# Optimization experiments

Hardware: AMD Instinct MI355X
Metric: run time of the kernel (lower is better)

Reference implementation:

```python
import jax, jax.numpy as jnp
import numpy as np

B, S, D, H = 8, 1024, 1024, 16
DK = D // H


def setup_inputs() -> dict:
    key = jax.random.key(0)
    ks = jax.random.split(key, 12)
    sc = 1.0 / np.sqrt(D)
    return {
        "query": jax.random.normal(ks[0], (B, S, D), jnp.float32),
        "key": jax.random.normal(ks[1], (B, S, D), jnp.float32),
        "value": jax.random.normal(ks[2], (B, S, D), jnp.float32),
        "Wq": jax.random.normal(ks[3], (D, D), jnp.float32) * sc,
        "bq": jnp.zeros((D,), jnp.float32),
        "Wk": jax.random.normal(ks[4], (D, D), jnp.float32) * sc,
        "bk": jnp.zeros((D,), jnp.float32),
        "Wv": jax.random.normal(ks[5], (D, D), jnp.float32) * sc,
        "bv": jnp.zeros((D,), jnp.float32),
        "Wa": jax.random.normal(ks[6], (D, D), jnp.float32) * sc,
        "ba": jnp.zeros((D,), jnp.float32),
        "qvec": jax.random.normal(ks[7], (D,), jnp.float32),
    }


def reference(query, key, value, Wq, bq, Wk, bk, Wv, bv, Wa, ba, qvec):
    # project and split heads: [B,S,D] -> [B,H,S,DK]
    def split(x, W, b):
        y = x @ W.T + b
        return y.reshape(B, S, H, DK).transpose(0, 2, 1, 3)

    q = split(query, Wq, bq)
    k = split(key, Wk, bk)
    v = split(value, Wv, bv)

    scores = jnp.einsum('bhqd,bhkd->bhqk', q, k) / jnp.sqrt(jnp.float32(DK))
    p = jax.nn.softmax(scores, axis=-1)          # dropout p=0 -> identity
    x = jnp.einsum('bhqk,bhkd->bhqd', p, v)
    x = x.transpose(0, 2, 1, 3).reshape(B, S, D)  # [B,S,D]

    # attention2 pooling head
    a = jnp.tanh(x @ Wa.T + ba) @ qvec           # [B,S]
    alpha = jax.nn.softmax(a, axis=-1)
    return jnp.einsum('bs,bsd->bd', alpha, x)    # [B,D]
```

## Files before the change

### kernel.cpp

```cpp
#include <hip/hip_runtime.h>

typedef __bf16 bf16;
typedef __attribute__((ext_vector_type(8))) __bf16 bf16x8;
typedef __attribute__((ext_vector_type(4))) __bf16 bf16x4;
typedef __attribute__((ext_vector_type(4))) float f32x4;

#define GLDS16(g, l) __builtin_amdgcn_global_load_lds( \
    (const __attribute__((address_space(1))) void*)(g), \
    (__attribute__((address_space(3))) void*)(l), 16, 0, 0)

#define MFMA16(a, b, c) __builtin_amdgcn_mfma_f32_16x16x32_bf16(a, b, c, 0, 0, 0)

#define TR16(dst, addr, off) \
  asm volatile("ds_read_b64_tr_b16 %0, %1 offset:" #off : "=v"(dst) : "v"(addr))

struct CvtAll { const float* in[7]; bf16* out[7]; };

__global__ __launch_bounds__(256) void f2b_all(CvtAll a) {
  const int i = blockIdx.x * 256 + threadIdx.x;
  const float* in;
  bf16* out;
  int off;
  if (blockIdx.y < 3) {
    in = a.in[blockIdx.y];
    out = a.out[blockIdx.y];
    off = i;
  } else {
    if (i >= 524288) return;
    const int widx = 3 + (i >> 17);
    in = a.in[widx];
    out = a.out[widx];
    off = i & 131071;
  }
  const f32x4* p = (const f32x4*)in + (size_t)off * 2;
  f32x4 x = p[0], y = p[1];
  bf16x8 o;
  o[0] = (bf16)x[0]; o[1] = (bf16)x[1]; o[2] = (bf16)x[2]; o[3] = (bf16)x[3];
  o[4] = (bf16)y[0]; o[5] = (bf16)y[1]; o[6] = (bf16)y[2]; o[7] = (bf16)y[3];
  ((bf16x8*)out)[off] = o;
}

template <int EPI, int MF>
__device__ __forceinline__ void gemm_body8(
    const bf16* __restrict__ A, const bf16* __restrict__ Bw,
    const float* __restrict__ bias, const float* __restrict__ qv,
    bf16* __restrict__ C, float* __restrict__ part,
    const int row0, const int col0, const int N, const int K) {
  constexpr int BM = MF * 32;
  constexpr int ASZ = MF * 1024;
  constexpr int BUF = 2 * ASZ + 16384;
  constexpr int RSH = (MF == 8) ? 8 : 7;
  __shared__ __attribute__((aligned(16))) bf16 L[2 * BUF];
  const int tid = threadIdx.x;
  const int wid = tid >> 6, lane = tid & 63;
  const int g = lane >> 4, lc = lane & 15;
  const int wr = wid >> 2, wc = wid & 3;

  const bf16* gA = A + (size_t)(row0 + (tid & (BM - 1))) * K + (tid >> RSH) * 8;
  const bf16* gB = Bw + (size_t)(col0 + (tid & 255)) * K + (tid >> 8) * 8;
  const int d0 = (tid - lane) * 8;

#define STG_A(T, kh) do { \
    const bf16* gp_ = gA + (T) * 64 + (kh) * 32; \
    bf16* lp_ = L + ((T) & 1) * BUF + (kh) * ASZ + d0; \
    GLDS16(gp_, lp_); \
    if constexpr (MF == 8) GLDS16(gp_ + 16, lp_ + 4096); } while (0)
#define STG_B(T, kh) do { \
    const bf16* gp_ = gB + (T) * 64 + (kh) * 32; \
    bf16* lp_ = L + ((T) & 1) * BUF + 2 * ASZ + (kh) * 8192 + d0; \
    GLDS16(gp_, lp_); GLDS16(gp_ + 16, lp_ + 4096); } while (0)
#define RD_A(c, kh) do { \
    _Pragma("unroll") for (int m_ = 0; m_ < MF; ++m_) \
      af[m_] = *(const bf16x8*)&L[(c) * BUF + (kh) * ASZ + g * (BM * 8) + \
                                  (wr * (MF * 16) + m_ * 16 + lc) * 8]; \
  } while (0)
#define RD_B(c, kh, nh) do { \
    bf[0] = *(const bf16x8*)&L[(c) * BUF + 2 * ASZ + (kh) * 8192 + g * 2048 + \
                               (wc * 64 + (nh) * 32 + lc) * 8]; \
    bf[1] = *(const bf16x8*)&L[(c) * BUF + 2 * ASZ + (kh) * 8192 + g * 2048 + \
                               (wc * 64 + (nh) * 32 + 16 + lc) * 8]; \
  } while (0)
#define BARS \
    __builtin_amdgcn_s_barrier(); \
    asm volatile("s_waitcnt lgkmcnt(0)" ::: "memory"); \
    __builtin_amdgcn_sched_barrier(0);
#define MM(nh) do { \
    __builtin_amdgcn_s_setprio(1); \
    _Pragma("unroll") for (int m_ = 0; m_ < MF; ++m_) { \
      acc[m_][(nh) * 2 + 0] = MFMA16(af[m_], bf[0], acc[m_][(nh) * 2 + 0]); \
      acc[m_][(nh) * 2 + 1] = MFMA16(af[m_], bf[1], acc[m_][(nh) * 2 + 1]); \
    } \
    __builtin_amdgcn_s_setprio(0); } while (0)
#define ENDP do { \
    __builtin_amdgcn_s_barrier(); \
    asm volatile("" ::: "memory"); \
    __builtin_amdgcn_sched_barrier(0); } while (0)
#define VGATE() do { \
    if constexpr (MF == 8) { asm volatile("s_waitcnt vmcnt(6)" ::: "memory"); } \
    else                   { asm volatile("s_waitcnt vmcnt(4)" ::: "memory"); } } while (0)

  const f32x4 z4 = {0.f, 0.f, 0.f, 0.f};
  f32x4 acc[MF][4];
#pragma unroll
  for (int m = 0; m < MF; ++m)
#pragma unroll
    for (int n = 0; n < 4; ++n) acc[m][n] = z4;

  bf16x8 af[MF], bf[2];
  const int NT = K >> 6;
  const int NI = NT >> 1;

  STG_A(0, 0); STG_B(0, 0); STG_A(0, 1); STG_B(0, 1);
  STG_A(1, 0); STG_B(1, 0); STG_A(1, 1);
  VGATE();
  ENDP;

  for (int i = 0; i < NI; ++i) {
    const int t1 = 2 * i + 1, t2 = 2 * i + 2, t3 = 2 * i + 3;
    const bool p2 = t2 < NT, p3 = t3 < NT;
    RD_A(0, 0); RD_B(0, 0, 0);
    STG_B(t1, 1);
    BARS; MM(0); ENDP;
    RD_B(0, 0, 1);
    if (p2) STG_A(t2, 0);
    BARS; MM(1); ENDP;
    RD_A(0, 1); RD_B(0, 1, 0);
    if (p2) STG_B(t2, 0);
    BARS; MM(0); ENDP;
    RD_B(0, 1, 1);
    if (p2) STG_A(t2, 1);
    BARS; MM(1);
    if (p2) { VGATE(); }
    else    { asm volatile("s_waitcnt vmcnt(0)" ::: "memory"); }
    ENDP;
    RD_A(1, 0); RD_B(1, 0, 0);
    if (p2) STG_B(t2, 1);
    BARS; MM(0); ENDP;
    RD_B(1, 0, 1);
    if (p3) STG_A(t3, 0);
    BARS; MM(1); ENDP;
    RD_A(1, 1); RD_B(1, 1, 0);
    if (p3) STG_B(t3, 0);
    BARS; MM(0); ENDP;
    RD_B(1, 1, 1);
    if (p3) STG_A(t3, 1);
    BARS; MM(1);
    VGATE();
    ENDP;
  }

#undef STG_A
#undef STG_B
#undef RD_A
#undef RD_B
#undef BARS
#undef MM
#undef ENDP
#undef VGATE

  if constexpr (EPI == 0) {
#pragma unroll
    for (int n = 0; n < 4; ++n) {
      const int col = col0 + wc * 64 + n * 16 + lc;
      const float bb = bias[col];
#pragma unroll
      for (int m = 0; m < MF; ++m)
#pragma unroll
        for (int r = 0; r < 4; ++r) {
          const int row = row0 + wr * (MF * 16) + m * 16 + g * 4 + r;
          C[(size_t)row * N + col] = (bf16)(acc[m][n][r] + bb);
        }
    }
  } else {
    float ps[MF][4];
#pragma unroll
    for (int m = 0; m < MF; ++m)
#pragma unroll
      for (int r = 0; r < 4; ++r) ps[m][r] = 0.f;
#pragma unroll
    for (int n = 0; n < 4; ++n) {
      const int col = col0 + wc * 64 + n * 16 + lc;
      const float bb = bias[col];
      const float qq = qv[col];
#pragma unroll
      for (int m = 0; m < MF; ++m)
#pragma unroll
        for (int r = 0; r < 4; ++r)
          ps[m][r] += tanhf(acc[m][n][r] + bb) * qq;
    }
    float* pdst = part + (size_t)((col0 >> 8) * 4 + wc) * 8192;
#pragma unroll
    for (int m = 0; m < MF; ++m)
#pragma unroll
      for (int r = 0; r < 4; ++r) {
        float v = ps[m][r];
        v += __shfl_xor(v, 1); v += __shfl_xor(v, 2);
        v += __shfl_xor(v, 4); v += __shfl_xor(v, 8);
        if (lc == 0) {
          const int row = row0 + wr * (MF * 16) + m * 16 + g * 4 + r;
          pdst[row] = v;
        }
      }
  }
}

__device__ __forceinline__ void swz128(int phys, int& row0, int& col0) {
  const int lg = (phys & 7) * 16 + (phys >> 3);
  row0 = (lg >> 2) * 256;
  col0 = (lg & 3) * 256;
}

__device__ __forceinline__ void swz256(int phys, int& row0, int& col0) {
  const int lg = (phys & 7) * 32 + (phys >> 3);
  row0 = (lg >> 2) * 128;
  col0 = (lg & 3) * 256;
}

struct GemmSet { const bf16* A; const bf16* Bw; const float* bias; bf16* C; };
struct Gemm3Args { GemmSet s[3]; };

__global__ __launch_bounds__(512, 2) void gemm3_kernel(Gemm3Args a) {
  const GemmSet s = a.s[blockIdx.y];
  int row0, col0;
  swz128(blockIdx.x, row0, col0);
  gemm_body8<0, 8>(s.A, s.Bw, s.bias, nullptr, s.C, nullptr, row0, col0, 1024, 1024);
}

__global__ __launch_bounds__(512, 2) void gemm_a_kernel(
    const bf16* __restrict__ A, const bf16* __restrict__ Bw,
    const float* __restrict__ bias, const float* __restrict__ qv,
    float* __restrict__ part) {
  int row0, col0;
  swz256(blockIdx.x, row0, col0);
  gemm_body8<1, 4>(A, Bw, bias, qv, nullptr, part, row0, col0, 1024, 1024);
}

__global__ __launch_bounds__(256) void attn_kernel(
    const bf16* __restrict__ qp, const bf16* __restrict__ kp,
    const bf16* __restrict__ vp, bf16* __restrict__ xb, float* __restrict__ xf) {
  constexpr int S = 1024, D = 1024;
  __shared__ __attribute__((aligned(16))) bf16 Ks[8192];
  __shared__ __attribute__((aligned(16))) bf16 Vs[8192];
  __shared__ __attribute__((aligned(16))) bf16 Ps[8192];
  const int tid = threadIdx.x, wid = tid >> 6, lane = tid & 63;
  const int g = lane >> 4, lc = lane & 15;
  const int b = blockIdx.x >> 4, h = blockIdx.x & 15;
  const int q0 = blockIdx.y * 128;
  const size_t base = (size_t)b * S * D + (size_t)h * 64;

  bf16x8 qf[2][2];
#pragma unroll
  for (int qg = 0; qg < 2; ++qg) {
    const bf16* qrow = qp + base + (size_t)(q0 + qg * 64 + wid * 16 + lc) * D;
    qf[qg][0] = *(const bf16x8*)(qrow + g * 8);
    qf[qg][1] = *(const bf16x8*)(qrow + 32 + g * 8);
#pragma unroll
    for (int j = 0; j < 8; ++j) {
      qf[qg][0][j] = (bf16)((float)qf[qg][0][j] * 0.125f);
      qf[qg][1][j] = (bf16)((float)qf[qg][1][j] * 0.125f);
    }
  }
  float m_s[2] = {-1e30f, -1e30f}, l_s[2] = {0.f, 0.f};
  const f32x4 z4 = {0.f, 0.f, 0.f, 0.f};
  f32x4 ax[2][4];
#pragma unroll
  for (int qg = 0; qg < 2; ++qg)
#pragma unroll
    for (int m = 0; m < 4; ++m) ax[qg][m] = z4;

  const int c0 = tid, c1 = tid + 256;
  const bf16* gK0 = kp + base + (size_t)(c0 & 63) * D + (c0 >> 6) * 8;
  const bf16* gK1 = kp + base + (size_t)(c1 & 63) * D + (c1 >> 6) * 8;
  bf16* lK0 = Ks + (size_t)(c0 - lane) * 8;
  bf16* lK1 = Ks + (size_t)(c1 - lane) * 8;
  const bf16* gV0 = vp + base + (size_t)((c0 >> 5) * 4 + ((c0 >> 1) & 3)) * D +
                    ((c0 >> 3) & 3) * 16 + (c0 & 1) * 8;
  const bf16* gV1 = vp + base + (size_t)((c1 >> 5) * 4 + ((c1 >> 1) & 3)) * D +
                    ((c1 >> 3) & 3) * 16 + (c1 & 1) * 8;
  bf16* lV0 = Vs + (size_t)(c0 - lane) * 8;
  bf16* lV1 = Vs + (size_t)(c1 - lane) * 8;

  bf16* pw = Ps + wid * 2048;
  const int pswz_a = lc & 3, pswz_b = (lc >> 2) & 3;
  const unsigned vaddr0 =
      (unsigned)(uintptr_t)(const __attribute__((address_space(3))) bf16*)(Vs + 512 * g + 4 * lc);

  GLDS16(gK0, lK0);
  GLDS16(gK1, lK1);
  GLDS16(gV0, lV0);
  GLDS16(gV1, lV1);

  for (int t = 0; t < 16; ++t) {
    __syncthreads();
    const int cur = t & 1;
    if (t < 15) {
      const size_t off = (size_t)(t + 1) * 64 * D;
      const int nb = cur ^ 1;
      GLDS16(gK0 + off, lK0 + nb * 4096);
      GLDS16(gK1 + off, lK1 + nb * 4096);
      GLDS16(gV0 + off, lV0 + nb * 4096);
      GLDS16(gV1 + off, lV1 + nb * 4096);
    }
    const bf16* Kb = Ks + cur * 4096;
    const unsigned va = vaddr0 + cur * 8192u;

    bf16x4 vt[4][2][2];
    TR16(vt[0][0][0], va, 0);    TR16(vt[1][0][0], va, 128);
    TR16(vt[2][0][0], va, 256);  TR16(vt[3][0][0], va, 384);
    TR16(vt[0][0][1], va, 512);  TR16(vt[1][0][1], va, 640);
    TR16(vt[2][0][1], va, 768);  TR16(vt[3][0][1], va, 896);
    TR16(vt[0][1][0], va, 4096); TR16(vt[1][1][0], va, 4224);
    TR16(vt[2][1][0], va, 4352); TR16(vt[3][1][0], va, 4480);
    TR16(vt[0][1][1], va, 4608); TR16(vt[1][1][1], va, 4736);
    TR16(vt[2][1][1], va, 4864); TR16(vt[3][1][1], va, 4992);
    asm volatile("s_waitcnt lgkmcnt(0)" ::: "memory");
    __builtin_amdgcn_sched_barrier(0);

#pragma unroll
    for (int qg = 0; qg < 2; ++qg) {
      f32x4 sc[4];
      __builtin_amdgcn_s_setprio(1);
#pragma unroll
      for (int m = 0; m < 4; ++m) {
        f32x4 z = z4;
        bf16x8 kf0 = *(const bf16x8*)(Kb + (size_t)g * 512 + (m * 16 + lc) * 8);
        bf16x8 kf1 = *(const bf16x8*)(Kb + (size_t)(4 + g) * 512 + (m * 16 + lc) * 8);
        z = MFMA16(kf0, qf[qg][0], z);
        z = MFMA16(kf1, qf[qg][1], z);
        sc[m] = z;
      }
      __builtin_amdgcn_s_setprio(0);

      float mx = -1e30f;
#pragma unroll
      for (int m = 0; m < 4; ++m)
        mx = fmaxf(mx, fmaxf(fmaxf(sc[m][0], sc[m][1]), fmaxf(sc[m][2], sc[m][3])));
      mx = fmaxf(mx, __shfl_xor(mx, 16));
      mx = fmaxf(mx, __shfl_xor(mx, 32));
      if (!__all(mx - m_s[qg] <= 8.f)) {
        const float mn = fmaxf(m_s[qg], mx);
        const float cr = __expf(m_s[qg] - mn);
        l_s[qg] *= cr;
#pragma unroll
        for (int m = 0; m < 4; ++m) ax[qg][m] *= cr;
        m_s[qg] = mn;
      }
      float sm = 0.f;
#pragma unroll
      for (int m = 0; m < 4; ++m)
#pragma unroll
        for (int r = 0; r < 4; ++r) {
          float p = __expf(sc[m][r] - m_s[qg]);
          sc[m][r] = p;
          sm += p;
        }
      sm += __shfl_xor(sm, 16);
      sm += __shfl_xor(sm, 32);
      l_s[qg] += sm;

      bf16* pg = pw + qg * 1024;
#pragma unroll
      for (int m = 0; m < 4; ++m) {
        bf16x4 pk;
        pk[0] = (bf16)sc[m][0]; pk[1] = (bf16)sc[m][1];
        pk[2] = (bf16)sc[m][2]; pk[3] = (bf16)sc[m][3];
        *(bf16x4*)(pg + lc * 64 + 16 * (m ^ pswz_a) + 4 * (g ^ pswz_b)) = pk;
      }

      bf16x4 pr[2][2];
#pragma unroll
      for (int kk = 0; kk < 2; ++kk)
#pragma unroll
        for (int jh = 0; jh < 2; ++jh) {
          const int msrc = 2 * kk + (g >> 1);
          const int gsrc = (2 * g + jh) & 3;
          pr[kk][jh] = *(const bf16x4*)(pg + lc * 64 + 16 * (msrc ^ pswz_a) + 4 * (gsrc ^ pswz_b));
        }
      bf16x8 pf0 = __builtin_shufflevector(pr[0][0], pr[0][1], 0, 1, 2, 3, 4, 5, 6, 7);
      bf16x8 pf1 = __builtin_shufflevector(pr[1][0], pr[1][1], 0, 1, 2, 3, 4, 5, 6, 7);

      __builtin_amdgcn_s_setprio(1);
#pragma unroll
      for (int md = 0; md < 4; ++md) {
        bf16x8 a0 = __builtin_shufflevector(vt[md][0][0], vt[md][0][1], 0, 1, 2, 3, 4, 5, 6, 7);
        bf16x8 a1 = __builtin_shufflevector(vt[md][1][0], vt[md][1][1], 0, 1, 2, 3, 4, 5, 6, 7);
        ax[qg][md] = MFMA16(a0, pf0, ax[qg][md]);
        ax[qg][md] = MFMA16(a1, pf1, ax[qg][md]);
      }
      __builtin_amdgcn_s_setprio(0);
    }
  }

#pragma unroll
  for (int qg = 0; qg < 2; ++qg) {
    const float inv = 1.0f / l_s[qg];
    const int qrow = q0 + qg * 64 + wid * 16 + lc;
    float* xfr = xf + base + (size_t)qrow * D;
    bf16* xbr = xb + base + (size_t)qrow * D;
#pragma unroll
    for (int m = 0; m < 4; ++m) {
      f32x4 vv = ax[qg][m] * inv;
      *(f32x4*)(xfr + 16 * m + 4 * g) = vv;
      bf16x4 bb;
      bb[0] = (bf16)vv[0]; bb[1] = (bf16)vv[1];
      bb[2] = (bf16)vv[2]; bb[3] = (bf16)vv[3];
      *(bf16x4*)(xbr + 16 * m + 4 * g) = bb;
    }
  }
}

__global__ __launch_bounds__(256) void softmax_part(const float* __restrict__ part,
                                                    float* __restrict__ alpha) {
  __shared__ float red[8];
  const int b = blockIdx.x, t = threadIdx.x;
  f32x4 a4 = {0.f, 0.f, 0.f, 0.f};
#pragma unroll
  for (int p = 0; p < 16; ++p) {
    const float* pp = part + (size_t)p * 8192 + b * 1024 + t * 4;
    a4[0] += pp[0]; a4[1] += pp[1]; a4[2] += pp[2]; a4[3] += pp[3];
  }
  float m = fmaxf(fmaxf(a4[0], a4[1]), fmaxf(a4[2], a4[3]));
#pragma unroll
  for (int o = 1; o < 64; o <<= 1) m = fmaxf(m, __shfl_xor(m, o));
  if ((t & 63) == 0) red[t >> 6] = m;
  __syncthreads();
  m = fmaxf(fmaxf(red[0], red[1]), fmaxf(red[2], red[3]));
  f32x4 e;
  float s = 0.f;
#pragma unroll
  for (int j = 0; j < 4; ++j) { e[j] = __expf(a4[j] - m); s += e[j]; }
#pragma unroll
  for (int o = 1; o < 64; o <<= 1) s += __shfl_xor(s, o);
  if ((t & 63) == 0) red[4 + (t >> 6)] = s;
  __syncthreads();
  const float inv = 1.0f / (red[4] + red[5] + red[6] + red[7]);
  *(f32x4*)(alpha + b * 1024 + t * 4) = e * inv;
}

__global__ __launch_bounds__(256) void pool_kernel(const float* __restrict__ xf,
                                                   const float* __restrict__ alpha,
                                                   float* __restrict__ out) {
  const int b = blockIdx.y, sc = blockIdx.x, t = threadIdx.x;
  f32x4 acc = {0.f, 0.f, 0.f, 0.f};
  const float* xrow = xf + (size_t)b * 1024 * 1024;
  for (int s = sc * 64; s < sc * 64 + 64; ++s) {
    const float al = alpha[b * 1024 + s];
    f32x4 xv = *(const f32x4*)(xrow + (size_t)s * 1024 + t * 4);
    acc += xv * al;
  }
  atomicAdd(&out[b * 1024 + t * 4 + 0], acc[0]);
  atomicAdd(&out[b * 1024 + t * 4 + 1], acc[1]);
  atomicAdd(&out[b * 1024 + t * 4 + 2], acc[2]);
  atomicAdd(&out[b * 1024 + t * 4 + 3], acc[3]);
}

extern "C" void kernel_launch(void* const* d_in, const int* in_sizes, int n_in,
                              void* d_out, int out_size, void* d_ws, size_t ws_size,
                              hipStream_t stream) {
  const float* Q   = (const float*)d_in[0];
  const float* K   = (const float*)d_in[1];
  const float* V   = (const float*)d_in[2];
  const float* Wq  = (const float*)d_in[3];
  const float* bq  = (const float*)d_in[4];
  const float* Wk  = (const float*)d_in[5];
  const float* bk  = (const float*)d_in[6];
  const float* Wv  = (const float*)d_in[7];
  const float* bv  = (const float*)d_in[8];
  const float* Wa  = (const float*)d_in[9];
  const float* ba  = (const float*)d_in[10];
  const float* qvec = (const float*)d_in[11];
  float* out = (float*)d_out;
  char* ws = (char*)d_ws;
  const size_t MB = 1ull << 20;

  bf16* Wqb = (bf16*)(ws + 0 * MB);
  bf16* Wkb = (bf16*)(ws + 2 * MB);
  bf16* Wvb = (bf16*)(ws + 4 * MB);
  bf16* Wab = (bf16*)(ws + 6 * MB);
  bf16* qb  = (bf16*)(ws + 8 * MB);
  bf16* kb  = (bf16*)(ws + 24 * MB);
  bf16* vb  = (bf16*)(ws + 40 * MB);
  bf16* qp  = (bf16*)(ws + 56 * MB);
  bf16* kp  = (bf16*)(ws + 72 * MB);
  bf16* vp  = (bf16*)(ws + 88 * MB);
  float* part  = (float*)(ws + 104 * MB);
  float* alpha = (float*)(ws + 104 * MB + 524288);
  bf16* xb  = qb;
  float* xf = (float*)(ws + 24 * MB);

  hipMemsetAsync(out, 0, 8192 * sizeof(float), stream);

  CvtAll cv = {{Q, K, V, Wq, Wk, Wv, Wa}, {qb, kb, vb, Wqb, Wkb, Wvb, Wab}};
  f2b_all<<<dim3(4096, 4), 256, 0, stream>>>(cv);

  Gemm3Args g3 = {{{qb, Wqb, bq, qp}, {kb, Wkb, bk, kp}, {vb, Wvb, bv, vp}}};
  gemm3_kernel<<<dim3(128, 3), 512, 0, stream>>>(g3);

  attn_kernel<<<dim3(128, 8), 256, 0, stream>>>(qp, kp, vp, xb, xf);

  gemm_a_kernel<<<256, 512, 0, stream>>>(xb, Wab, ba, qvec, part);

  softmax_part<<<8, 256, 0, stream>>>(part, alpha);
  pool_kernel<<<dim3(16, 8), 256, 0, stream>>>(xf, alpha, out);
}
```

Before: 246.2 us.

## Restructure GEMM main loop into four phases with full-width B fragment reads

The GEMM mainloop now loads all four B fragments per phase and issues a full MFMA block of MF×4 per barrier pair, instead of splitting each k-half into two half-N phases. This halves the number of barrier-separated phases per iteration and regroups the A/B global-to-LDS staging. The vmcnt wait thresholds are adjusted to match. The aim is to cut barrier and synchronisation overhead and give larger MFMA bursts between barriers. The cost is more live B registers, and the reworked staging and wait counts risk hazards if the gating is wrong.

New measurement: 252.6 us. +2.6%, slower.

```diff
diff --git a/kernel.cpp b/kernel.cpp
--- a/kernel.cpp
+++ b/kernel.cpp
@@ -74,30 +74,33 @@
       af[m_] = *(const bf16x8*)&L[(c) * BUF + (kh) * ASZ + g * (BM * 8) + \
                                   (wr * (MF * 16) + m_ * 16 + lc) * 8]; \
   } while (0)
-#define RD_B(c, kh, nh) do { \
-    bf[0] = *(const bf16x8*)&L[(c) * BUF + 2 * ASZ + (kh) * 8192 + g * 2048 + \
-                               (wc * 64 + (nh) * 32 + lc) * 8]; \
-    bf[1] = *(const bf16x8*)&L[(c) * BUF + 2 * ASZ + (kh) * 8192 + g * 2048 + \
-                               (wc * 64 + (nh) * 32 + 16 + lc) * 8]; \
+#define RD_B4(c, kh) do { \
+    const int bb_ = (c) * BUF + 2 * ASZ + (kh) * 8192 + g * 2048; \
+    bf[0] = *(const bf16x8*)&L[bb_ + (wc * 64 + 0 + lc) * 8]; \
+    bf[1] = *(const bf16x8*)&L[bb_ + (wc * 64 + 16 + lc) * 8]; \
+    bf[2] = *(const bf16x8*)&L[bb_ + (wc * 64 + 32 + lc) * 8]; \
+    bf[3] = *(const bf16x8*)&L[bb_ + (wc * 64 + 48 + lc) * 8]; \
   } while (0)
 #define BARS \
     __builtin_amdgcn_s_barrier(); \
     asm volatile("s_waitcnt lgkmcnt(0)" ::: "memory"); \
     __builtin_amdgcn_sched_barrier(0);
-#define MM(nh) do { \
+#define MM4() do { \
     __builtin_amdgcn_s_setprio(1); \
     _Pragma("unroll") for (int m_ = 0; m_ < MF; ++m_) { \
-      acc[m_][(nh) * 2 + 0] = MFMA16(af[m_], bf[0], acc[m_][(nh) * 2 + 0]); \
-      acc[m_][(nh) * 2 + 1] = MFMA16(af[m_], bf[1], acc[m_][(nh) * 2 + 1]); \
+      acc[m_][0] = MFMA16(af[m_], bf[0], acc[m_][0]); \
+      acc[m_][1] = MFMA16(af[m_], bf[1], acc[m_][1]); \
+      acc[m_][2] = MFMA16(af[m_], bf[2], acc[m_][2]); \
+      acc[m_][3] = MFMA16(af[m_], bf[3], acc[m_][3]); \
     } \
     __builtin_amdgcn_s_setprio(0); } while (0)
 #define ENDP do { \
     __builtin_amdgcn_s_barrier(); \
     asm volatile("" ::: "memory"); \
     __builtin_amdgcn_sched_barrier(0); } while (0)
-#define VGATE() do { \
-    if constexpr (MF == 8) { asm volatile("s_waitcnt vmcnt(6)" ::: "memory"); } \
-    else                   { asm volatile("s_waitcnt vmcnt(4)" ::: "memory"); } } while (0)
+#define VG() do { \
+    if constexpr (MF == 8) { asm volatile("s_waitcnt vmcnt(8)" ::: "memory"); } \
+    else                   { asm volatile("s_waitcnt vmcnt(6)" ::: "memory"); } } while (0)
 
   const f32x4 z4 = {0.f, 0.f, 0.f, 0.f};
   f32x4 acc[MF][4];
@@ -106,57 +109,44 @@
 #pragma unroll
     for (int n = 0; n < 4; ++n) acc[m][n] = z4;
 
-  bf16x8 af[MF], bf[2];
+  bf16x8 af[MF], bf[4];
   const int NT = K >> 6;
   const int NI = NT >> 1;
 
   STG_A(0, 0); STG_B(0, 0); STG_A(0, 1); STG_B(0, 1);
-  STG_A(1, 0); STG_B(1, 0); STG_A(1, 1);
-  VGATE();
+  STG_A(1, 0); STG_B(1, 0);
+  if constexpr (MF == 8) { asm volatile("s_waitcnt vmcnt(4)" ::: "memory"); }
+  else                   { asm volatile("s_waitcnt vmcnt(3)" ::: "memory"); }
   ENDP;
 
   for (int i = 0; i < NI; ++i) {
     const int t1 = 2 * i + 1, t2 = 2 * i + 2, t3 = 2 * i + 3;
-    const bool p2 = t2 < NT, p3 = t3 < NT;
-    RD_A(0, 0); RD_B(0, 0, 0);
-    STG_B(t1, 1);
-    BARS; MM(0); ENDP;
-    RD_B(0, 0, 1);
-    if (p2) STG_A(t2, 0);
-    BARS; MM(1); ENDP;
-    RD_A(0, 1); RD_B(0, 1, 0);
-    if (p2) STG_B(t2, 0);
-    BARS; MM(0); ENDP;
-    RD_B(0, 1, 1);
-    if (p2) STG_A(t2, 1);
-    BARS; MM(1);
-    if (p2) { VGATE(); }
+    const bool p2 = t2 < NT;
+    RD_A(0, 0); RD_B4(0, 0);
+    STG_A(t1, 1); STG_B(t1, 1);
+    BARS; MM4(); VG(); ENDP;
+    RD_A(0, 1); RD_B4(0, 1);
+    if (p2) { STG_A(t2, 0); STG_B(t2, 0); }
+    BARS; MM4(); VG(); ENDP;
+    RD_A(1, 0); RD_B4(1, 0);
+    if (p2) { STG_A(t2, 1); STG_B(t2, 1); }
+    BARS; MM4();
+    if (p2) { VG(); }
     else    { asm volatile("s_waitcnt vmcnt(0)" ::: "memory"); }
     ENDP;
-    RD_A(1, 0); RD_B(1, 0, 0);
-    if (p2) STG_B(t2, 1);
-    BARS; MM(0); ENDP;
-    RD_B(1, 0, 1);
-    if (p3) STG_A(t3, 0);
-    BARS; MM(1); ENDP;
-    RD_A(1, 1); RD_B(1, 1, 0);
-    if (p3) STG_B(t3, 0);
-    BARS; MM(0); ENDP;
-    RD_B(1, 1, 1);
-    if (p3) STG_A(t3, 1);
-    BARS; MM(1);
-    VGATE();
-    ENDP;
+    RD_A(1, 1); RD_B4(1, 1);
+    if (p2) { STG_A(t3, 0); STG_B(t3, 0); }
+    BARS; MM4(); VG(); ENDP;
   }
 
 #undef STG_A
 #undef STG_B
 #undef RD_A
-#undef RD_B
+#undef RD_B4
 #undef BARS
-#undef MM
+#undef MM4
 #undef ENDP
-#undef VGATE
+#undef VG
 
   if constexpr (EPI == 0) {
 #pragma unroll
```
